# Optimization experiments

Measured on AMD Instinct MI355X. Metric: run time of the kernel, lower is better.

Reference implementation:

```python
import jax, jax.numpy as jnp
import numpy as np

EPS = 1e-5


def _gcn_norm(edge_index, N):
    # symmetric GCN normalization with self-loops: D^-1/2 (A+I) D^-1/2
    row, col = edge_index[0], edge_index[1]
    loop = jnp.arange(N, dtype=row.dtype)
    row_f = jnp.concatenate([row, loop])
    col_f = jnp.concatenate([col, loop])
    deg = jax.ops.segment_sum(jnp.ones_like(row_f, dtype=jnp.float32), row_f, num_segments=N)
    dinv = jnp.where(deg > 0, jax.lax.rsqrt(jnp.maximum(deg, 1.0)), 0.0)
    norm = dinv[row_f] * dinv[col_f]  # [E+N]
    return row_f, col_f, norm


def _gcn_conv(h, W, b, row_f, col_f, norm, N):
    h = h @ W  # [N, C_out] small GEMM
    msg = h[col_f] * norm[:, None]  # gather over edges  [E+N, C_out]
    return jax.ops.segment_sum(msg, row_f, num_segments=N) + b


def _bn_eval(h, gamma, beta, mean, var):
    return (h - mean) * jax.lax.rsqrt(var + EPS) * gamma + beta


def setup_inputs() -> dict:
    key = jax.random.key(0)
    ks = jax.random.split(key, 12)
    N, E = 100000, 1600000
    C_in, C_hid, C_out = 64, 64, 64
    x = jax.random.normal(ks[0], (N, C_in), dtype=jnp.float32)
    edge_index = jax.random.randint(ks[1], (2, E), 0, N, dtype=jnp.int32)
    s = 1.0 / np.sqrt(C_hid)
    inp = {
        "x": x,
        "edge_index": edge_index,
        "W1": jax.random.normal(ks[2], (C_in, C_hid), dtype=jnp.float32) * s,
        "b1": jnp.zeros((C_hid,), jnp.float32),
        "g1": jnp.ones((C_hid,), jnp.float32),
        "be1": jnp.zeros((C_hid,), jnp.float32),
        "m1": jax.random.normal(ks[3], (C_hid,), dtype=jnp.float32) * 0.1,
        "v1": jax.random.uniform(ks[4], (C_hid,), minval=0.5, maxval=1.5, dtype=jnp.float32),
        "W2": jax.random.normal(ks[5], (C_hid, C_hid), dtype=jnp.float32) * s,
        "b2": jnp.zeros((C_hid,), jnp.float32),
        "g2": jnp.ones((C_hid,), jnp.float32),
        "be2": jnp.zeros((C_hid,), jnp.float32),
        "m2": jax.random.normal(ks[6], (C_hid,), dtype=jnp.float32) * 0.1,
        "v2": jax.random.uniform(ks[7], (C_hid,), minval=0.5, maxval=1.5, dtype=jnp.float32),
        "W3": jax.random.normal(ks[8], (C_hid, C_out), dtype=jnp.float32) * s,
        "b3": jnp.zeros((C_out,), jnp.float32),
    }
    return inp


def reference(x, edge_index, W1, b1, g1, be1, m1, v1, W2, b2, g2, be2, m2, v2, W3, b3):
    N = x.shape[0]
    row_f, col_f, norm = _gcn_norm(edge_index, N)  # cached=True: computed once
    h = _gcn_conv(x, W1, b1, row_f, col_f, norm, N)
    h = jax.nn.relu(_bn_eval(h, g1, be1, m1, v1))  # dropout off (eval)
    h = _gcn_conv(h, W2, b2, row_f, col_f, norm, N)
    h = jax.nn.relu(_bn_eval(h, g2, be2, m2, v2))
    global_embeddings = h
    hc_predictions = _gcn_conv(global_embeddings, W3, b3, row_f, col_f, norm, N)
    return (global_embeddings, hc_predictions)
```

## Files before the change

### kernel.cpp

```cpp
#include <hip/hip_runtime.h>

typedef __attribute__((ext_vector_type(8))) short bfrag8;
typedef __attribute__((ext_vector_type(4))) float facc4;
typedef __attribute__((ext_vector_type(8))) unsigned short u16x8;

#define CROWS  256
#define NCBMAX 512
#define CAP    8192
#define CHUNK  4096
#define SLACK  772
#define BPITCH (CAP + SLACK)

static __device__ __forceinline__ float bf2f(ushort u) {
    union { unsigned int i; float f; } x;
    x.i = ((unsigned int)u) << 16;
    return x.f;
}
static __device__ __forceinline__ ushort f2bf(float f) {
    union { float f; unsigned int i; } x;
    x.f = f;
    unsigned int r = x.i + 0x7FFFu + ((x.i >> 16) & 1u);
    return (ushort)(r >> 16);
}

__global__ void k_prep(const float* __restrict__ W1, const float* __restrict__ W2,
                       const float* __restrict__ W3,
                       const float* __restrict__ b1, const float* __restrict__ g1,
                       const float* __restrict__ be1, const float* __restrict__ m1,
                       const float* __restrict__ v1,
                       const float* __restrict__ b2, const float* __restrict__ g2,
                       const float* __restrict__ be2, const float* __restrict__ m2,
                       const float* __restrict__ v2,
                       const float* __restrict__ b3,
                       ushort* __restrict__ wp, float* __restrict__ pp) {
    int l = blockIdx.x;
    const float* W = (l == 0) ? W1 : (l == 1) ? W2 : W3;
    ushort* wo = wp + l * 4096;
    for (int idx = threadIdx.x; idx < 4096; idx += blockDim.x) {
        int j = idx & 7, m = (idx >> 3) & 15, quad = (idx >> 7) & 3;
        int ks = (idx >> 9) & 1, c2 = idx >> 10;
        wo[idx] = f2bf(W[(32 * ks + 8 * quad + j) * 64 + c2 * 16 + m]);
    }
    if (threadIdx.x < 64) {
        int ch = threadIdx.x;
        float PS, PH;
        if (l == 0) {
            float sc = g1[ch] * rsqrtf(v1[ch] + 1e-5f);
            PS = sc; PH = be1[ch] - m1[ch] * sc + b1[ch] * sc;
        } else if (l == 1) {
            float sc = g2[ch] * rsqrtf(v2[ch] + 1e-5f);
            PS = sc; PH = be2[ch] - m2[ch] * sc + b2[ch] * sc;
        } else {
            PS = 1.f; PH = b3[ch];
        }
        pp[l * 128 + ch] = PS;
        pp[l * 128 + 64 + ch] = PH;
    }
}


__global__ void k_cinit(int* __restrict__ ccur, int ncb,
                        ushort* __restrict__ ta, ushort* __restrict__ tb, int N) {
    int b = blockIdx.x * blockDim.x + threadIdx.x;
    if (b < ncb) ccur[b] = b * CAP;
    if (blockIdx.x == 0 && threadIdx.x < 64) {
        ta[(size_t)N * 64 + threadIdx.x] = 0;
        tb[(size_t)N * 64 + threadIdx.x] = 0;
    }
}

__global__ void k_part(const int* __restrict__ row, const int* __restrict__ col, int E,
                       int* __restrict__ ccur, int* __restrict__ bkt, int ncb) {
    __shared__ int recs[CHUNK];
    __shared__ unsigned short cbl[CHUNK];
    __shared__ int hist[NCBMAX], lbase[NCBMAX], loff[NCBMAX];
    int tid = threadIdx.x;
    int chunk0 = blockIdx.x * CHUNK;
    for (int i = tid; i < ncb; i += blockDim.x) hist[i] = 0;
    __syncthreads();
    for (int j = tid; j < CHUNK; j += blockDim.x) {
        int e = chunk0 + j;
        if (e < E) {
            int r = row[e];
            int cb = r >> 8;
            recs[j] = ((r & (CROWS - 1)) << 17) | col[e];
            cbl[j] = (unsigned short)cb;
            atomicAdd(&hist[cb], 1);
        } else cbl[j] = 0xFFFF;
    }
    __syncthreads();
    for (int i = tid; i < ncb; i += blockDim.x) {
        int h = hist[i];
        lbase[i] = h ? atomicAdd(&ccur[i], h) : 0;
        loff[i] = 0;
    }
    __syncthreads();
    for (int j = tid; j < CHUNK; j += blockDim.x) {
        unsigned short cb = cbl[j];
        if (cb != 0xFFFF) {
            int p = lbase[cb] + atomicAdd(&loff[cb], 1);
            if (p < (cb + 1) * CAP) bkt[p] = recs[j];
        }
    }
}

__global__ void k_build(const int* __restrict__ bkt, const int* __restrict__ ccur,
                        int* __restrict__ rptr, int* __restrict__ deg,
                        float* __restrict__ dinv, int* __restrict__ cidx, int N) {
    __shared__ int hist[CROWS], wstart[CROWS], cur[CROWS], psum[CROWS];
    int tid = threadIdx.x;
    int b = blockIdx.x;
    int lo = b * CROWS;
    int nr = min(CROWS, N - lo);
    int in0 = b * CAP;
    int cntE = min(ccur[b] - in0, CAP);
    int out0 = b * BPITCH;

    if (tid < CROWS) hist[tid] = 0;
    __syncthreads();
    for (int i = tid; i < cntE; i += blockDim.x)
        atomicAdd(&hist[bkt[in0 + i] >> 17], 1);
    __syncthreads();
    int d = 0, ep = 0;
    if (tid < CROWS) {
        d = hist[tid];
        ep = (d + 3) & ~3;
        psum[tid] = ep;
    }
    __syncthreads();
    #pragma unroll
    for (int off = 1; off < CROWS; off <<= 1) {
        int t = (tid >= off && tid < CROWS) ? psum[tid - off] : 0;
        __syncthreads();
        if (tid < CROWS) psum[tid] += t;
        __syncthreads();
    }
    if (tid < CROWS) {
        int ws = out0 + psum[tid] - ep;
        wstart[tid] = ws;
        cur[tid] = ws;
        if (tid < nr) {
            rptr[lo + tid] = ws;
            deg[lo + tid] = d;
            dinv[lo + tid] = rsqrtf((float)(d + 1));
        }
    }
    __syncthreads();
    for (int i = tid; i < cntE; i += blockDim.x) {
        int v = bkt[in0 + i];
        int p = atomicAdd(&cur[v >> 17], 1);
        cidx[p] = v & 0x1FFFF;
    }
    __syncthreads();
    if (tid < nr) {
        int dd = hist[tid];
        int epp = (dd + 3) & ~3;
        for (int j = dd; j < epp; j++) cidx[wstart[tid] + j] = N;
    }
}

__global__ void k_gemm(const float* __restrict__ Hv, const ushort* __restrict__ wq,
                       const float* __restrict__ dinv,
                       ushort* __restrict__ T, int ntiles, int N) {
    int lane = threadIdx.x & 63;
    int wid = (blockIdx.x * blockDim.x + threadIdx.x) >> 6;
    int nw = (gridDim.x * blockDim.x) >> 6;
    int m = lane & 15, quad = lane >> 4;

    bfrag8 bf[2][4];
    #pragma unroll
    for (int s = 0; s < 2; s++)
        #pragma unroll
        for (int c = 0; c < 4; c++)
            bf[s][c] = *(const bfrag8*)(wq +
                (size_t)((((c * 2 + s) * 4 + quad) * 16 + m) * 8));

    for (int t = wid; t < ntiles; t += nw) {
        int nodeA = t * 16 + m;
        if (nodeA >= N) nodeA = N - 1;
        bfrag8 a0, a1;
        const float* arow = Hv + (size_t)nodeA * 64;
        #pragma unroll
        for (int s = 0; s < 2; s++) {
            float4 u0 = *(const float4*)(arow + s * 32 + quad * 8);
            float4 u1 = *(const float4*)(arow + s * 32 + quad * 8 + 4);
            bfrag8 f;
            f[0] = (short)f2bf(u0.x); f[1] = (short)f2bf(u0.y);
            f[2] = (short)f2bf(u0.z); f[3] = (short)f2bf(u0.w);
            f[4] = (short)f2bf(u1.x); f[5] = (short)f2bf(u1.y);
            f[6] = (short)f2bf(u1.z); f[7] = (short)f2bf(u1.w);
            if (s == 0) a0 = f; else a1 = f;
        }
        facc4 acc[4];
        #pragma unroll
        for (int c = 0; c < 4; c++) { acc[c][0]=0.f; acc[c][1]=0.f; acc[c][2]=0.f; acc[c][3]=0.f; }
        #pragma unroll
        for (int c = 0; c < 4; c++) {
            acc[c] = __builtin_amdgcn_mfma_f32_16x16x32_bf16(a0, bf[0][c], acc[c], 0, 0, 0);
            acc[c] = __builtin_amdgcn_mfma_f32_16x16x32_bf16(a1, bf[1][c], acc[c], 0, 0, 0);
        }
        #pragma unroll
        for (int c = 0; c < 4; c++)
            #pragma unroll
            for (int r = 0; r < 4; r++) {
                int node = t * 16 + quad * 4 + r;
                if (node < N)
                    T[(size_t)node * 64 + c * 16 + m] = f2bf(dinv[node] * acc[c][r]);
            }
    }
}

template <bool FUSE>
__global__ void __launch_bounds__(256, 6)
k_aggf(const ushort* __restrict__ T2, const int* __restrict__ rptr,
       const int* __restrict__ deg, const float* __restrict__ dinv,
       const int* __restrict__ cidx,
       const float* __restrict__ pp, int relu,
       const ushort* __restrict__ wq,
       float* __restrict__ outf, ushort* __restrict__ Tn, int N) {
    __shared__ ushort lds_h[32][72];

    int tid = threadIdx.x;
    int lane = tid & 63;
    int wl = tid >> 6;
    int grp = lane >> 3;
    int s = lane & 7;
    int loc = wl * 8 + grp;
    int r = blockIdx.x * 32 + loc;
    bool rv = (r < N);
    int rs = rv ? r : N;

    int start = rv ? rptr[r] : 0;
    int ep = rv ? ((deg[r] + 3) & ~3) : 0;
    u16x8 sf = *(const u16x8*)(T2 + (size_t)rs * 64 + s * 8);
    float dr = rv ? dinv[r] : 0.f;

    float a[8];
    #pragma unroll
    for (int k = 0; k < 8; k++) a[k] = 0.f;

    int i = 0;
    bool have8 = (8 <= ep);
    int4 c4, d4;
    if (have8) {
        c4 = *(const int4*)(cidx + start);
        d4 = *(const int4*)(cidx + start + 4);
    }
    while (have8) {
        int ni = i + 8;
        bool nhave = (ni + 8 <= ep);
        int4 nc4, nd4;
        if (nhave) {
            nc4 = *(const int4*)(cidx + start + ni);
            nd4 = *(const int4*)(cidx + start + ni + 4);
        }
        u16x8 t0 = *(const u16x8*)(T2 + (size_t)c4.x * 64 + s * 8);
        u16x8 t1 = *(const u16x8*)(T2 + (size_t)c4.y * 64 + s * 8);
        u16x8 t2 = *(const u16x8*)(T2 + (size_t)c4.z * 64 + s * 8);
        u16x8 t3 = *(const u16x8*)(T2 + (size_t)c4.w * 64 + s * 8);
        u16x8 t4 = *(const u16x8*)(T2 + (size_t)d4.x * 64 + s * 8);
        u16x8 t5 = *(const u16x8*)(T2 + (size_t)d4.y * 64 + s * 8);
        u16x8 t6 = *(const u16x8*)(T2 + (size_t)d4.z * 64 + s * 8);
        u16x8 t7 = *(const u16x8*)(T2 + (size_t)d4.w * 64 + s * 8);
        #pragma unroll
        for (int k = 0; k < 8; k++)
            a[k] += ((bf2f(t0[k]) + bf2f(t1[k])) + (bf2f(t2[k]) + bf2f(t3[k]))) +
                    ((bf2f(t4[k]) + bf2f(t5[k])) + (bf2f(t6[k]) + bf2f(t7[k])));
        c4 = nc4; d4 = nd4; i = ni; have8 = nhave;
    }
    if (i < ep) {
        int4 e4 = *(const int4*)(cidx + start + i);
        u16x8 t0 = *(const u16x8*)(T2 + (size_t)e4.x * 64 + s * 8);
        u16x8 t1 = *(const u16x8*)(T2 + (size_t)e4.y * 64 + s * 8);
        u16x8 t2 = *(const u16x8*)(T2 + (size_t)e4.z * 64 + s * 8);
        u16x8 t3 = *(const u16x8*)(T2 + (size_t)e4.w * 64 + s * 8);
        #pragma unroll
        for (int k = 0; k < 8; k++)
            a[k] += (bf2f(t0[k]) + bf2f(t1[k])) + (bf2f(t2[k]) + bf2f(t3[k]));
    }

    float4 ps0 = *(const float4*)(pp + s * 8);
    float4 ps1 = *(const float4*)(pp + s * 8 + 4);
    float4 ph0 = *(const float4*)(pp + 64 + s * 8);
    float4 ph1 = *(const float4*)(pp + 64 + s * 8 + 4);
    float PS[8] = {ps0.x, ps0.y, ps0.z, ps0.w, ps1.x, ps1.y, ps1.z, ps1.w};
    float PH[8] = {ph0.x, ph0.y, ph0.z, ph0.w, ph1.x, ph1.y, ph1.z, ph1.w};

    float v[8];
    #pragma unroll
    for (int k = 0; k < 8; k++) v[k] = 0.f;
    if (rv) {
        #pragma unroll
        for (int k = 0; k < 8; k++) {
            v[k] = dr * (a[k] + bf2f(sf[k])) * PS[k] + PH[k];
            if (relu) v[k] = fmaxf(v[k], 0.f);
        }
        if (outf) {
            *(float4*)(outf + (size_t)r * 64 + s * 8) = make_float4(v[0], v[1], v[2], v[3]);
            *(float4*)(outf + (size_t)r * 64 + s * 8 + 4) = make_float4(v[4], v[5], v[6], v[7]);
        }
    }

    if constexpr (FUSE) {
        u16x8 hv;
        #pragma unroll
        for (int k = 0; k < 8; k++) hv[k] = rv ? f2bf(v[k]) : (ushort)0;
        *(u16x8*)&lds_h[loc][s * 8] = hv;

        int m = lane & 15, quad = lane >> 4;
        int rtile = wl >> 1, chalf = wl & 1;
        bfrag8 bw[2][2];
        #pragma unroll
        for (int ks = 0; ks < 2; ks++)
            #pragma unroll
            for (int c = 0; c < 2; c++)
                bw[ks][c] = *(const bfrag8*)(wq +
                    (size_t)(((((chalf * 2 + c) * 2 + ks) * 4 + quad) * 16 + m) * 8));
        __syncthreads();

        bfrag8 a0 = *(const bfrag8*)&lds_h[rtile * 16 + m][quad * 8];
        bfrag8 a1 = *(const bfrag8*)&lds_h[rtile * 16 + m][32 + quad * 8];
        facc4 acc[2];
        #pragma unroll
        for (int c = 0; c < 2; c++) { acc[c][0]=0.f; acc[c][1]=0.f; acc[c][2]=0.f; acc[c][3]=0.f; }
        #pragma unroll
        for (int c = 0; c < 2; c++) {
            acc[c] = __builtin_amdgcn_mfma_f32_16x16x32_bf16(a0, bw[0][c], acc[c], 0, 0, 0);
            acc[c] = __builtin_amdgcn_mfma_f32_16x16x32_bf16(a1, bw[1][c], acc[c], 0, 0, 0);
        }
        int nodeBase = blockIdx.x * 32 + rtile * 16;
        #pragma unroll
        for (int c = 0; c < 2; c++)
            #pragma unroll
            for (int rr = 0; rr < 4; rr++) {
                int node = nodeBase + quad * 4 + rr;
                if (node < N)
                    Tn[(size_t)node * 64 + (chalf * 2 + c) * 16 + m] =
                        f2bf(dinv[node] * acc[c][rr]);
            }
    }
}


extern "C" void kernel_launch(void* const* d_in, const int* in_sizes, int n_in,
                              void* d_out, int out_size, void* d_ws, size_t ws_size,
                              hipStream_t stream) {
    const float* x  = (const float*)d_in[0];
    const int*   ei = (const int*)d_in[1];
    const float *W1 = (const float*)d_in[2],  *b1 = (const float*)d_in[3];
    const float *g1 = (const float*)d_in[4],  *be1= (const float*)d_in[5];
    const float *m1 = (const float*)d_in[6],  *v1 = (const float*)d_in[7];
    const float *W2 = (const float*)d_in[8],  *b2 = (const float*)d_in[9];
    const float *g2 = (const float*)d_in[10], *be2= (const float*)d_in[11];
    const float *m2 = (const float*)d_in[12], *v2 = (const float*)d_in[13];
    const float *W3 = (const float*)d_in[14], *b3 = (const float*)d_in[15];

    int N = in_sizes[0] / 64;
    int E = in_sizes[1] / 2;
    const int* row = ei;
    const int* col = ei + E;
    int ncb = (N + CROWS - 1) / CROWS;

    char* p = (char*)d_ws;
    auto take = [&](size_t b) -> char* {
        char* q = p;
        p += (b + 255) & ~(size_t)255;
        return q;
    };
    int*    ccur  = (int*)   take((size_t)ncb * 4);
    int*    rptr  = (int*)   take((size_t)N * 4);
    int*    deg   = (int*)   take((size_t)N * 4);
    float*  dinv  = (float*) take((size_t)N * 4);
    ushort* wp    = (ushort*)take((size_t)3 * 4096 * 2);
    float*  pp    = (float*) take((size_t)3 * 128 * 4);
    int*    bkt   = (int*)   take((size_t)ncb * CAP * 4);
    int*    cidx  = (int*)   take((size_t)ncb * BPITCH * 4 + 1024);
    ushort* ta    = (ushort*)take((size_t)(N + 1) * 64 * 2);
    ushort* tb    = (ushort*)take((size_t)(N + 1) * 64 * 2);

    const int TB = 256;
    const int TBP = 1024;
    int nchunks = (E + CHUNK - 1) / CHUNK;
    k_prep <<<3, TB, 0, stream>>>(W1, W2, W3, b1, g1, be1, m1, v1,
                                  b2, g2, be2, m2, v2, b3, wp, pp);
    k_cinit<<<(ncb + TB - 1) / TB, TB, 0, stream>>>(ccur, ncb, ta, tb, N);
    k_part <<<nchunks, TBP, 0, stream>>>(row, col, E, ccur, bkt, ncb);
    k_build<<<ncb, TBP, 0, stream>>>(bkt, ccur, rptr, deg, dinv, cidx, N);

    float* outp = (float*)d_out;
    int ntiles = (N + 15) >> 4;
    int GG = (ntiles + 3) / 4;
    int GA = (N + 31) / 32;

    k_gemm<<<GG, TB, 0, stream>>>(x, wp, dinv, ta, ntiles, N);
    k_aggf<true><<<GA, TB, 0, stream>>>(ta, rptr, deg, dinv, cidx, pp, 1,
                                        wp + 4096, (float*)nullptr, tb, N);
    k_aggf<true><<<GA, TB, 0, stream>>>(tb, rptr, deg, dinv, cidx, pp + 128, 1,
                                        wp + 8192, outp, ta, N);
    k_aggf<false><<<GA, TB, 0, stream>>>(ta, rptr, deg, dinv, cidx, pp + 256, 0,
                                         (const ushort*)nullptr,
                                         outp + (size_t)N * 64, (ushort*)nullptr, N);
}
```

Measured before the change: 258.9 us.

## Coalesce edge partition scatter via shared-memory local sort and fuse init into prep

k_part now computes a shared-memory prefix scan over per-bucket histograms and reorders chunk records into bucket order in LDS before writing, so global stores to the bucket array are contiguous runs instead of scattered writes. The separate counter/pad initialization kernel is folded into k_prep as an extra block, removing one launch. The cost is roughly double the shared memory in k_part and extra barriers in the scan, which may reduce occupancy.

```diff
diff --git a/kernel.cpp b/kernel.cpp
--- a/kernel.cpp
+++ b/kernel.cpp
@@ -32,40 +32,40 @@
                        const float* __restrict__ be2, const float* __restrict__ m2,
                        const float* __restrict__ v2,
                        const float* __restrict__ b3,
-                       ushort* __restrict__ wp, float* __restrict__ pp) {
+                       ushort* __restrict__ wp, float* __restrict__ pp,
+                       int* __restrict__ ccur, int ncb,
+                       ushort* __restrict__ ta, ushort* __restrict__ tb, int N) {
     int l = blockIdx.x;
-    const float* W = (l == 0) ? W1 : (l == 1) ? W2 : W3;
-    ushort* wo = wp + l * 4096;
-    for (int idx = threadIdx.x; idx < 4096; idx += blockDim.x) {
-        int j = idx & 7, m = (idx >> 3) & 15, quad = (idx >> 7) & 3;
-        int ks = (idx >> 9) & 1, c2 = idx >> 10;
-        wo[idx] = f2bf(W[(32 * ks + 8 * quad + j) * 64 + c2 * 16 + m]);
-    }
-    if (threadIdx.x < 64) {
-        int ch = threadIdx.x;
-        float PS, PH;
-        if (l == 0) {
-            float sc = g1[ch] * rsqrtf(v1[ch] + 1e-5f);
-            PS = sc; PH = be1[ch] - m1[ch] * sc + b1[ch] * sc;
-        } else if (l == 1) {
-            float sc = g2[ch] * rsqrtf(v2[ch] + 1e-5f);
-            PS = sc; PH = be2[ch] - m2[ch] * sc + b2[ch] * sc;
-        } else {
-            PS = 1.f; PH = b3[ch];
-        }
-        pp[l * 128 + ch] = PS;
-        pp[l * 128 + 64 + ch] = PH;
-    }
-}
-
-
-__global__ void k_cinit(int* __restrict__ ccur, int ncb,
-                        ushort* __restrict__ ta, ushort* __restrict__ tb, int N) {
-    int b = blockIdx.x * blockDim.x + threadIdx.x;
-    if (b < ncb) ccur[b] = b * CAP;
-    if (blockIdx.x == 0 && threadIdx.x < 64) {
-        ta[(size_t)N * 64 + threadIdx.x] = 0;
-        tb[(size_t)N * 64 + threadIdx.x] = 0;
+    if (l < 3) {
+        const float* W = (l == 0) ? W1 : (l == 1) ? W2 : W3;
+        ushort* wo = wp + l * 4096;
+        for (int idx = threadIdx.x; idx < 4096; idx += blockDim.x) {
+            int j = idx & 7, m = (idx >> 3) & 15, quad = (idx >> 7) & 3;
+            int ks = (idx >> 9) & 1, c2 = idx >> 10;
+            wo[idx] = f2bf(W[(32 * ks + 8 * quad + j) * 64 + c2 * 16 + m]);
+        }
+        if (threadIdx.x < 64) {
+            int ch = threadIdx.x;
+            float PS, PH;
+            if (l == 0) {
+                float sc = g1[ch] * rsqrtf(v1[ch] + 1e-5f);
+                PS = sc; PH = be1[ch] - m1[ch] * sc + b1[ch] * sc;
+            } else if (l == 1) {
+                float sc = g2[ch] * rsqrtf(v2[ch] + 1e-5f);
+                PS = sc; PH = be2[ch] - m2[ch] * sc + b2[ch] * sc;
+            } else {
+                PS = 1.f; PH = b3[ch];
+            }
+            pp[l * 128 + ch] = PS;
+            pp[l * 128 + 64 + ch] = PH;
+        }
+    } else {
+        for (int b = threadIdx.x; b < ncb; b += blockDim.x) ccur[b] = b * CAP;
+        if (threadIdx.x < 128) {
+            int t = threadIdx.x;
+            if (t < 64) ta[(size_t)N * 64 + t] = 0;
+            else        tb[(size_t)N * 64 + (t - 64)] = 0;
+        }
     }
 }
 
@@ -73,20 +73,21 @@
                        int* __restrict__ ccur, int* __restrict__ bkt, int ncb) {
     __shared__ int recs[CHUNK];
     __shared__ unsigned short cbl[CHUNK];
-    __shared__ int hist[NCBMAX], lbase[NCBMAX], loff[NCBMAX];
+    __shared__ int recs2[CHUNK];
+    __shared__ int gofs[CHUNK];
+    __shared__ int hist[NCBMAX], lbase[NCBMAX], loff[NCBMAX], lpos[NCBMAX];
     int tid = threadIdx.x;
     int chunk0 = blockIdx.x * CHUNK;
-    for (int i = tid; i < ncb; i += blockDim.x) hist[i] = 0;
-    __syncthreads();
-    for (int j = tid; j < CHUNK; j += blockDim.x) {
-        int e = chunk0 + j;
-        if (e < E) {
-            int r = row[e];
-            int cb = r >> 8;
-            recs[j] = ((r & (CROWS - 1)) << 17) | col[e];
-            cbl[j] = (unsigned short)cb;
-            atomicAdd(&hist[cb], 1);
-        } else cbl[j] = 0xFFFF;
+    int cnt = min(CHUNK, E - chunk0);
+
+    for (int i = tid; i < NCBMAX; i += blockDim.x) { hist[i] = 0; }
+    __syncthreads();
+    for (int j = tid; j < cnt; j += blockDim.x) {
+        int r = row[chunk0 + j];
+        int cb = r >> 8;
+        recs[j] = ((r & (CROWS - 1)) << 17) | col[chunk0 + j];
+        cbl[j] = (unsigned short)cb;
+        atomicAdd(&hist[cb], 1);
     }
     __syncthreads();
     for (int i = tid; i < ncb; i += blockDim.x) {
@@ -94,13 +95,27 @@
         lbase[i] = h ? atomicAdd(&ccur[i], h) : 0;
         loff[i] = 0;
     }
-    __syncthreads();
-    for (int j = tid; j < CHUNK; j += blockDim.x) {
-        unsigned short cb = cbl[j];
-        if (cb != 0xFFFF) {
-            int p = lbase[cb] + atomicAdd(&loff[cb], 1);
-            if (p < (cb + 1) * CAP) bkt[p] = recs[j];
-        }
+    if (tid < NCBMAX) lpos[tid] = hist[tid];
+    __syncthreads();
+    #pragma unroll
+    for (int off = 1; off < NCBMAX; off <<= 1) {
+        int t = (tid < NCBMAX && tid >= off) ? lpos[tid - off] : 0;
+        __syncthreads();
+        if (tid < NCBMAX) lpos[tid] += t;
+        __syncthreads();
+    }
+    for (int j = tid; j < cnt; j += blockDim.x) {
+        int cb = cbl[j];
+        int p = atomicAdd(&loff[cb], 1);
+        int lp = lpos[cb] - hist[cb] + p;
+        recs2[lp] = recs[j];
+        int gp = lbase[cb] + p;
+        gofs[lp] = (gp < (cb + 1) * CAP) ? gp : -1;
+    }
+    __syncthreads();
+    for (int t = tid; t < cnt; t += blockDim.x) {
+        int g = gofs[t];
+        if (g >= 0) bkt[g] = recs2[t];
     }
 }
 
@@ -381,9 +396,9 @@
     const int TB = 256;
     const int TBP = 1024;
     int nchunks = (E + CHUNK - 1) / CHUNK;
-    k_prep <<<3, TB, 0, stream>>>(W1, W2, W3, b1, g1, be1, m1, v1,
-                                  b2, g2, be2, m2, v2, b3, wp, pp);
-    k_cinit<<<(ncb + TB - 1) / TB, TB, 0, stream>>>(ccur, ncb, ta, tb, N);
+    k_prep <<<4, TB, 0, stream>>>(W1, W2, W3, b1, g1, be1, m1, v1,
+                                  b2, g2, be2, m2, v2, b3, wp, pp,
+                                  ccur, ncb, ta, tb, N);
     k_part <<<nchunks, TBP, 0, stream>>>(row, col, E, ccur, bkt, ncb);
     k_build<<<ncb, TBP, 0, stream>>>(bkt, ccur, rptr, deg, dinv, cidx, N);
 
```

Result: no change. 255.0 us (-1.5%).
